# Kernel tuning notes

Hardware: AMD Instinct MI355X
Metric: run time of the kernel (lower is better)

The kernel has to match this reference:

```python
import jax, jax.numpy as jnp
import numpy as np

NH, NKV, HD = 32, 8, 128      # query heads, kv heads, head dim
B, S, H = 4, 1024, 4096       # batch, per-seq tokens (prefill, no history), hidden
BLOCK = 64                    # paged KV-cache block size
BPS = S // BLOCK              # blocks per sequence


def rotate_half(x):
    x1, x2 = jnp.split(x, 2, axis=-1)
    return jnp.concatenate([-x2, x1], axis=-1)


def setup_inputs() -> dict:
    key = jax.random.key(0)
    ks = jax.random.split(key, 5)
    hidden_states = jax.random.normal(ks[0], (B * S, H), jnp.float32)
    Wq = jax.random.normal(ks[1], (H, NH * HD), jnp.float32) * 0.02
    Wk = jax.random.normal(ks[2], (H, NKV * HD), jnp.float32) * 0.02
    Wv = jax.random.normal(ks[3], (H, NKV * HD), jnp.float32) * 0.02
    Wo = jax.random.normal(ks[4], (NH * HD, H), jnp.float32) * 0.02
    # standard llama rope inverse frequencies
    inv_freq = 1.0 / (10000.0 ** (jnp.arange(0, HD, 2, dtype=jnp.float32) / HD))
    # empty paged KV cache: [num_blocks, block, n_kv_heads, head_dim]
    k_cache = jnp.zeros((B * BPS, BLOCK, NKV, HD), jnp.float32)
    v_cache = jnp.zeros((B * BPS, BLOCK, NKV, HD), jnp.float32)
    # per-token positions (prefill, history=0): 0..S-1 for each sequence
    position_ids_1d = jnp.tile(jnp.arange(S, dtype=jnp.int32), B)
    # block table: which cache block holds each logical block of each sequence
    block_offsets = jnp.arange(B * BPS, dtype=jnp.int32).reshape(B, BPS)
    return dict(hidden_states=hidden_states, Wq=Wq, Wk=Wk, Wv=Wv, Wo=Wo,
                inv_freq=inv_freq, k_cache=k_cache, v_cache=v_cache,
                position_ids_1d=position_ids_1d, block_offsets=block_offsets)


def reference(hidden_states, Wq, Wk, Wv, Wo, inv_freq, k_cache, v_cache,
              position_ids_1d, block_offsets):
    # qkv projections (contiguous-batching: tokens flattened)
    q = (hidden_states @ Wq).reshape(-1, NH, HD)
    k = (hidden_states @ Wk).reshape(-1, NKV, HD)
    v = (hidden_states @ Wv).reshape(-1, NKV, HD)

    # fused rotary: cos/sin from inv_freq at per-token 1d positions
    freqs = position_ids_1d.astype(jnp.float32)[:, None] * inv_freq[None, :]  # [T, HD/2]
    emb = jnp.concatenate([freqs, freqs], axis=-1)                            # [T, HD]
    cos = jnp.cos(emb)[:, None, :]
    sin = jnp.sin(emb)[:, None, :]
    q = q * cos + rotate_half(q) * sin
    k = k * cos + rotate_half(k) * sin

    # fill_kv_cache: scatter rotated K / raw V into paged cache via block_offsets
    flat_offsets = block_offsets.reshape(-1)
    k_blk = k.reshape(B * BPS, BLOCK, NKV, HD)
    v_blk = v.reshape(B * BPS, BLOCK, NKV, HD)
    k_cache = k_cache.at[flat_offsets].set(k_blk)
    v_cache = v_cache.at[flat_offsets].set(v_blk)

    # paged_attention_fwd: gather K/V blocks back via block table
    kk = k_cache[block_offsets].reshape(B, BPS * BLOCK, NKV, HD)  # [B, Skv, NKV, HD]
    vv = v_cache[block_offsets].reshape(B, BPS * BLOCK, NKV, HD)
    groups = NH // NKV
    kk = jnp.repeat(kk, groups, axis=2)  # repeat_kv -> [B, Skv, NH, HD]
    vv = jnp.repeat(vv, groups, axis=2)

    qb = q.reshape(B, S, NH, HD)
    scale = 1.0 / jnp.sqrt(jnp.float32(HD))
    scores = jnp.einsum('bqhd,bkhd->bhqk', qb, kk) * scale  # [B, NH, S, Skv]
    causal = jnp.arange(S)[:, None] >= jnp.arange(BPS * BLOCK)[None, :]
    scores = jnp.where(causal[None, None], scores, jnp.float32(-1e30))
    probs = jax.nn.softmax(scores, axis=-1)
    attn = jnp.einsum('bhqk,bkhd->bqhd', probs, vv).reshape(B * S, NH * HD)
    return attn @ Wo
```

## Files before the change

kernel.cpp:

```cpp
#include <hip/hip_runtime.h>
#include <cstdint>
#include <cstddef>


typedef unsigned short u16;
typedef __bf16 bf16x8 __attribute__((ext_vector_type(8)));
typedef float  f32x4  __attribute__((ext_vector_type(4)));

#define SEQ 1024
#define QKV_COLS 6144
#define NHEAD 32
#define NKVH 8
#define HDIM 128

__device__ __forceinline__ u16 f2bf(float f) {
  union { float f; uint32_t u; } v; v.f = f;
  return (u16)((v.u + 0x7fffu + ((v.u >> 16) & 1u)) >> 16);
}
__device__ __forceinline__ float bf2f(u16 x) {
  union { uint32_t u; float f; } v; v.u = ((uint32_t)x) << 16;
  return v.f;
}

typedef __attribute__((address_space(1))) const uint32_t g_u32;
typedef __attribute__((address_space(3))) uint32_t l_u32;
__device__ __forceinline__ void async_copy16(const u16* g, u16* lds_base) {
  __builtin_amdgcn_global_load_lds((g_u32*)g, (l_u32*)lds_base, 16, 0, 0);
}

__global__ void cast_f32_bf16(const float* __restrict__ in, u16* __restrict__ out, int n) {
  int i = (blockIdx.x * 256 + threadIdx.x) * 4;
  if (i >= n) return;
  float4 v = *(const float4*)&in[i];
  uint2 pk;
  pk.x = (uint32_t)f2bf(v.x) | ((uint32_t)f2bf(v.y) << 16);
  pk.y = (uint32_t)f2bf(v.z) | ((uint32_t)f2bf(v.w) << 16);
  *(uint2*)&out[i] = pk;
}

__global__ void transpose_f32_bf16(const float* __restrict__ in, u16* __restrict__ out,
                                   int R, int C) {
  __shared__ float tile[32][33];
  int c0 = blockIdx.x * 32, r0 = blockIdx.y * 32;
  int tx = threadIdx.x, ty = threadIdx.y;
  tile[ty][tx] = in[(size_t)(r0 + ty) * C + c0 + tx];
  __syncthreads();
  out[(size_t)(c0 + ty) * R + r0 + tx] = f2bf(tile[tx][ty]);
}

template <int MODE>
__global__ __launch_bounds__(512, 2) void gemm_bt(const u16* __restrict__ A,
                                                  const u16* __restrict__ Bt,
                                                  void* __restrict__ Cv,
                                                  u16* __restrict__ Vt,
                                                  int M, int N, int K, int ldc,
                                                  int nbx) {
  __shared__ __align__(16) u16 smem[4][2][256 * 32];

  const int tid = threadIdx.x;
  const int lane = tid & 63, wave = tid >> 6;
  const int l15 = lane & 15, qd = lane >> 4;
  const int wm = wave >> 2, wn = wave & 3;

  const int nwg = gridDim.x;
  const int bid = (int)blockIdx.x;
  const int swz = (bid & 7) * (nwg >> 3) + (bid >> 3);
  const int bx = swz % nbx, by = swz / nbx;
  const int row0 = by * 256, col0 = bx * 256;

  const int sl = (qd ^ (l15 & 3) ^ (l15 >> 2)) * 8;

  int soff[2], cb[2];
#pragma unroll
  for (int call = 0; call < 2; ++call) {
    const int c = call * 512 + tid;
    const int r = c >> 2, j = c & 3;
    const int src = j ^ (r & 3) ^ ((r >> 2) & 3);
    soff[call] = r * K + src * 8;
    cb[call] = (call * 512 + wave * 64) * 8;
  }

  const u16* Ab = A + (size_t)row0 * K;
  const u16* Bb = Bt + (size_t)col0 * K;
  const int NT = K >> 5;

  f32x4 acc[8][4] = {};

#pragma unroll
  for (int tt = 0; tt < 3; ++tt) {
#pragma unroll
    for (int call = 0; call < 2; ++call)
      async_copy16(&Ab[tt * 32 + soff[call]], &smem[tt][0][cb[call]]);
#pragma unroll
    for (int call = 0; call < 2; ++call)
      async_copy16(&Bb[tt * 32 + soff[call]], &smem[tt][1][cb[call]]);
  }
  asm volatile("s_waitcnt vmcnt(4)" ::: "memory");
  __builtin_amdgcn_s_barrier();
  asm volatile("" ::: "memory");

  bf16x8 a0[4], b0[4];
#pragma unroll
  for (int i = 0; i < 4; ++i) {
    a0[i] = *(const bf16x8*)&smem[0][0][(wm * 128 + i * 16 + l15) * 32 + sl];
    b0[i] = *(const bf16x8*)&smem[0][1][(wn * 64 + i * 16 + l15) * 32 + sl];
  }

#pragma unroll 2
  for (int t = 0; t < NT; ++t) {
    const int bsel = t & 3, nsel = (t + 1) & 3, ssel = (t + 3) & 3;
    const bool do_stage = (t + 3) < NT;
    const int knext = (t + 3) * 32;

    bf16x8 a1[4];
#pragma unroll
    for (int i = 0; i < 4; ++i)
      a1[i] = *(const bf16x8*)&smem[bsel][0][(wm * 128 + 64 + i * 16 + l15) * 32 + sl];
    if (do_stage) {
#pragma unroll
      for (int call = 0; call < 2; ++call)
        async_copy16(&Ab[knext + soff[call]], &smem[ssel][0][cb[call]]);
    }
    __builtin_amdgcn_sched_barrier(0);
    __builtin_amdgcn_s_setprio(1);
#pragma unroll
    for (int mi = 0; mi < 4; ++mi)
#pragma unroll
      for (int ni = 0; ni < 4; ++ni)
        acc[mi][ni] = __builtin_amdgcn_mfma_f32_16x16x32_bf16(a0[mi], b0[ni], acc[mi][ni], 0, 0, 0);
    __builtin_amdgcn_s_setprio(0);

    bf16x8 a2[4], b2[4];
    if (t + 1 < NT) {
#pragma unroll
      for (int i = 0; i < 4; ++i) {
        a2[i] = *(const bf16x8*)&smem[nsel][0][(wm * 128 + i * 16 + l15) * 32 + sl];
        b2[i] = *(const bf16x8*)&smem[nsel][1][(wn * 64 + i * 16 + l15) * 32 + sl];
      }
    }
    if (do_stage) {
#pragma unroll
      for (int call = 0; call < 2; ++call)
        async_copy16(&Bb[knext + soff[call]], &smem[ssel][1][cb[call]]);
    }
    __builtin_amdgcn_sched_barrier(0);
    __builtin_amdgcn_s_setprio(1);
#pragma unroll
    for (int mi = 0; mi < 4; ++mi)
#pragma unroll
      for (int ni = 0; ni < 4; ++ni)
        acc[4 + mi][ni] = __builtin_amdgcn_mfma_f32_16x16x32_bf16(a1[mi], b0[ni], acc[4 + mi][ni], 0, 0, 0);
    __builtin_amdgcn_s_setprio(0);

    if (t < NT - 2) {
      if (t < NT - 3) asm volatile("s_waitcnt vmcnt(4)" ::: "memory");
      else            asm volatile("s_waitcnt vmcnt(0)" ::: "memory");
      __builtin_amdgcn_s_barrier();
      asm volatile("" ::: "memory");
    }
#pragma unroll
    for (int i = 0; i < 4; ++i) { a0[i] = a2[i]; b0[i] = b2[i]; }
  }

  if (MODE == 0 && col0 >= 5120) {
#pragma unroll
    for (int mi = 0; mi < 8; ++mi)
#pragma unroll
      for (int ni = 0; ni < 4; ++ni) {
        const int col = col0 + wn * 64 + ni * 16 + l15;
        const int dcol = col - 5120, kvh = dcol >> 7, d = dcol & 127;
        const int row = row0 + wm * 128 + mi * 16 + qd * 4;
        const int bb = row >> 10, p = row & 1023;
        ushort4 pk;
        pk.x = f2bf(acc[mi][ni][0]); pk.y = f2bf(acc[mi][ni][1]);
        pk.z = f2bf(acc[mi][ni][2]); pk.w = f2bf(acc[mi][ni][3]);
        *(ushort4*)&Vt[(((size_t)(bb * 8 + kvh) * 128) + d) * 1024 + p] = pk;
      }
    return;
  }
#pragma unroll
  for (int mi = 0; mi < 8; ++mi)
#pragma unroll
    for (int ni = 0; ni < 4; ++ni)
#pragma unroll
      for (int r = 0; r < 4; ++r) {
        int row = row0 + wm * 128 + mi * 16 + qd * 4 + r;
        int col = col0 + wn * 64 + ni * 16 + l15;
        float v = acc[mi][ni][r];
        if (MODE == 1) ((float*)Cv)[(size_t)row * ldc + col] = v;
        else           ((u16*)Cv)[(size_t)row * ldc + col] = f2bf(v);
      }
}

__global__ void rope_kernel(u16* __restrict__ qkv, const float* __restrict__ inv_freq,
                            const int* __restrict__ pos) {
  int idx = blockIdx.x * 256 + threadIdx.x;
  int t = idx / 2560;
  int r = idx - t * 2560;
  int hh = r >> 6, i = r & 63;
  float f = (float)pos[t] * inv_freq[i];
  float s, c;
  sincosf(f, &s, &c);
  size_t base = (size_t)t * QKV_COLS + hh * HDIM + i;
  float x1 = bf2f(qkv[base]), x2 = bf2f(qkv[base + 64]);
  qkv[base]      = f2bf(x1 * c - x2 * s);
  qkv[base + 64] = f2bf(x2 * c + x1 * s);
}

__global__ __launch_bounds__(512, 4) void attn_kernel(const u16* __restrict__ qkv,
                                                      const u16* __restrict__ vt,
                                                      u16* __restrict__ ao) {
  __shared__ __align__(16) u16 Ks[64 * 136];
  __shared__ __align__(16) u16 Vts[128 * 68];
  __shared__ __align__(16) u16 Ps[8][16 * 68];

  const int tid = threadIdx.x;
  const int lane = tid & 63, wave = tid >> 6;
  const int l15 = lane & 15, qd = lane >> 4;
  const int qt = blockIdx.x, h = blockIdx.y, b = blockIdx.z;
  const int q0 = qt * 128;
  const int kvh = h >> 2;
  const float scale = 0.08838834764831845f;

  bf16x8 qf[4];
  {
    const size_t qrow = (size_t)(b * SEQ + q0 + wave * 16 + l15) * QKV_COLS + h * HDIM;
#pragma unroll
    for (int s = 0; s < 4; ++s) qf[s] = *(const bf16x8*)&qkv[qrow + s * 32 + qd * 8];
  }

  f32x4 o[8] = {};
  float mrow[4] = {-__builtin_inff(), -__builtin_inff(), -__builtin_inff(), -__builtin_inff()};
  float lrow[4] = {0.f, 0.f, 0.f, 0.f};

  const int nkt = qt * 2 + 2;
  const size_t vbase0 = ((size_t)(b * NKVH + kvh) * HDIM) * SEQ;
  for (int kt = 0; kt < nkt; ++kt) {
    const int kv0 = kt * 64;
#pragma unroll
    for (int rnd = 0; rnd < 2; ++rnd) {
      int c = tid + rnd * 512;
      int kv = c >> 4, dc = (c & 15) * 8;
      *(uint4*)&Ks[kv * 136 + dc] =
          *(const uint4*)&qkv[(size_t)(b * SEQ + kv0 + kv) * QKV_COLS + 4096 + kvh * HDIM + dc];
    }
#pragma unroll
    for (int rnd = 0; rnd < 2; ++rnd) {
      int c = tid + rnd * 512;
      int d = c >> 3, kc = (c & 7) * 8;
      *(uint4*)&Vts[d * 68 + kc] = *(const uint4*)&vt[vbase0 + (size_t)d * SEQ + kv0 + kc];
    }
    __syncthreads();

    f32x4 st[4] = {};
#pragma unroll
    for (int t = 0; t < 4; ++t)
#pragma unroll
      for (int s = 0; s < 4; ++s) {
        bf16x8 kf = *(const bf16x8*)&Ks[(t * 16 + l15) * 136 + s * 32 + qd * 8];
        st[t] = __builtin_amdgcn_mfma_f32_16x16x32_bf16(qf[s], kf, st[t], 0, 0, 0);
      }

    float al[4];
#pragma unroll
    for (int r = 0; r < 4; ++r) {
      const int qpos = q0 + wave * 16 + qd * 4 + r;
      float sc[4];
#pragma unroll
      for (int t = 0; t < 4; ++t) {
        sc[t] = st[t][r] * scale;
        if (kv0 + t * 16 + l15 > qpos) sc[t] = -1e30f;
      }
      float mt = fmaxf(fmaxf(sc[0], sc[1]), fmaxf(sc[2], sc[3]));
      mt = fmaxf(mt, __shfl_xor(mt, 8));
      mt = fmaxf(mt, __shfl_xor(mt, 4));
      mt = fmaxf(mt, __shfl_xor(mt, 2));
      mt = fmaxf(mt, __shfl_xor(mt, 1));
      const float mn = fmaxf(mrow[r], mt);
      al[r] = __expf(mrow[r] - mn);
      float p[4], rs = 0.f;
#pragma unroll
      for (int t = 0; t < 4; ++t) { p[t] = __expf(sc[t] - mn); rs += p[t]; }
      rs += __shfl_xor(rs, 8);
      rs += __shfl_xor(rs, 4);
      rs += __shfl_xor(rs, 2);
      rs += __shfl_xor(rs, 1);
      lrow[r] = lrow[r] * al[r] + rs;
      mrow[r] = mn;
#pragma unroll
      for (int t = 0; t < 4; ++t)
        Ps[wave][(qd * 4 + r) * 68 + t * 16 + l15] = f2bf(p[t]);
    }
    asm volatile("s_waitcnt lgkmcnt(0)" ::: "memory");

    {
      const int srcl = (l15 >> 2) * 16;
      float a0 = __shfl(al[0], srcl), a1 = __shfl(al[1], srcl);
      float a2 = __shfl(al[2], srcl), a3 = __shfl(al[3], srcl);
      const int rr = l15 & 3;
      float aq = (rr & 2) ? ((rr & 1) ? a3 : a2) : ((rr & 1) ? a1 : a0);
#pragma unroll
      for (int dt = 0; dt < 8; ++dt) o[dt] *= aq;
    }
    {
      const bf16x8 pf0 = *(const bf16x8*)&Ps[wave][l15 * 68 + qd * 8];
      const bf16x8 pf1 = *(const bf16x8*)&Ps[wave][l15 * 68 + 32 + qd * 8];
#pragma unroll
      for (int dt = 0; dt < 8; ++dt) {
        const bf16x8 vf0 = *(const bf16x8*)&Vts[(dt * 16 + l15) * 68 + qd * 8];
        const bf16x8 vf1 = *(const bf16x8*)&Vts[(dt * 16 + l15) * 68 + 32 + qd * 8];
        o[dt] = __builtin_amdgcn_mfma_f32_16x16x32_bf16(vf0, pf0, o[dt], 0, 0, 0);
        o[dt] = __builtin_amdgcn_mfma_f32_16x16x32_bf16(vf1, pf1, o[dt], 0, 0, 0);
      }
    }
    __syncthreads();
  }

  {
    const int srcl = (l15 >> 2) * 16;
    float l0 = __shfl(lrow[0], srcl), l1 = __shfl(lrow[1], srcl);
    float l2 = __shfl(lrow[2], srcl), l3 = __shfl(lrow[3], srcl);
    const int rr = l15 & 3;
    float lq = (rr & 2) ? ((rr & 1) ? l3 : l2) : ((rr & 1) ? l1 : l0);
    const float inv = 1.0f / lq;
    const size_t obase = (size_t)(b * SEQ + q0 + wave * 16 + l15) * (NHEAD * HDIM) + h * HDIM;
#pragma unroll
    for (int dt = 0; dt < 8; ++dt) {
      ushort4 pk;
      pk.x = f2bf(o[dt][0] * inv); pk.y = f2bf(o[dt][1] * inv);
      pk.z = f2bf(o[dt][2] * inv); pk.w = f2bf(o[dt][3] * inv);
      *(ushort4*)&ao[obase + dt * 16 + qd * 4] = pk;
    }
  }
}

extern "C" void kernel_launch(void* const* d_in, const int* in_sizes, int n_in,
                              void* d_out, int out_size, void* d_ws, size_t ws_size,
                              hipStream_t stream) {
  const float* X    = (const float*)d_in[0];
  const float* Wq   = (const float*)d_in[1];
  const float* Wk   = (const float*)d_in[2];
  const float* Wv   = (const float*)d_in[3];
  const float* Wo   = (const float*)d_in[4];
  const float* invf = (const float*)d_in[5];
  const int*   pos  = (const int*)d_in[8];
  float* out = (float*)d_out;

  char* ws = (char*)d_ws;
  u16* Xbf   = (u16*)(ws + 0);
  u16* Wqkvt = (u16*)(ws + 33554432);
  u16* Wot   = (u16*)(ws + 83886080);
  u16* QKV   = (u16*)(ws + 117440512);
  u16* Vt    = (u16*)(ws + 167772160);
  u16* AO    = Xbf;

  dim3 tb32(32, 32);
  cast_f32_bf16<<<16384, 256, 0, stream>>>(X, Xbf, 16777216);
  transpose_f32_bf16<<<dim3(128, 128), tb32, 0, stream>>>(Wq, Wqkvt, 4096, 4096);
  transpose_f32_bf16<<<dim3(32, 128),  tb32, 0, stream>>>(Wk, Wqkvt + (size_t)4096 * 4096, 4096, 1024);
  transpose_f32_bf16<<<dim3(32, 128),  tb32, 0, stream>>>(Wv, Wqkvt + (size_t)5120 * 4096, 4096, 1024);
  transpose_f32_bf16<<<dim3(128, 128), tb32, 0, stream>>>(Wo, Wot, 4096, 4096);

  gemm_bt<0><<<dim3(24 * 16), 512, 0, stream>>>(Xbf, Wqkvt, QKV, Vt, 4096, 6144, 4096, 6144, 24);
  rope_kernel<<<40960, 256, 0, stream>>>(QKV, invf, pos);
  attn_kernel<<<dim3(8, 32, 4), 512, 0, stream>>>(QKV, Vt, AO);
  gemm_bt<1><<<dim3(16 * 16), 512, 0, stream>>>(AO, Wot, out, Vt, 4096, 4096, 4096, 4096, 16);
}
```

Before: 812.1 us.

## Fuse RoPE into QKV GEMM epilogue by retiling waves to cover full head dims

The GEMM wave layout changes from 2x4 (128 rows x 64 cols per wave) to 4x2 (64 rows x 128 cols per wave), so each wave holds a full 128-wide head and its rotate-half partner columns in registers. RoPE is then applied in the QKV GEMM epilogue using __sincosf, and the separate rope_kernel launch with its extra read-modify-write pass over Q/K is removed. The MFMA/LDS-read interleaving is reorganised to match the new tiling. The trade-offs are the less precise fast sincos, the transcendental work added to the epilogue, and a changed LDS read pattern.

```diff
diff --git a/kernel.cpp b/kernel.cpp
--- a/kernel.cpp
+++ b/kernel.cpp
@@ -53,6 +53,8 @@
                                                   const u16* __restrict__ Bt,
                                                   void* __restrict__ Cv,
                                                   u16* __restrict__ Vt,
+                                                  const float* __restrict__ invf,
+                                                  const int* __restrict__ pos,
                                                   int M, int N, int K, int ldc,
                                                   int nbx) {
   __shared__ __align__(16) u16 smem[4][2][256 * 32];
@@ -60,7 +62,7 @@
   const int tid = threadIdx.x;
   const int lane = tid & 63, wave = tid >> 6;
   const int l15 = lane & 15, qd = lane >> 4;
-  const int wm = wave >> 2, wn = wave & 3;
+  const int wm = wave & 3, wn = wave >> 2;
 
   const int nwg = gridDim.x;
   const int bid = (int)blockIdx.x;
@@ -84,7 +86,7 @@
   const u16* Bb = Bt + (size_t)col0 * K;
   const int NT = K >> 5;
 
-  f32x4 acc[8][4] = {};
+  f32x4 acc[4][8] = {};
 
 #pragma unroll
   for (int tt = 0; tt < 3; ++tt) {
@@ -99,23 +101,57 @@
   __builtin_amdgcn_s_barrier();
   asm volatile("" ::: "memory");
 
-  bf16x8 a0[4], b0[4];
+  bf16x8 a[4], b[4];
 #pragma unroll
   for (int i = 0; i < 4; ++i) {
-    a0[i] = *(const bf16x8*)&smem[0][0][(wm * 128 + i * 16 + l15) * 32 + sl];
-    b0[i] = *(const bf16x8*)&smem[0][1][(wn * 64 + i * 16 + l15) * 32 + sl];
+    a[i] = *(const bf16x8*)&smem[0][0][(wm * 64 + i * 16 + l15) * 32 + sl];
+    b[i] = *(const bf16x8*)&smem[0][1][(wn * 128 + i * 16 + l15) * 32 + sl];
   }
 
 #pragma unroll 2
   for (int t = 0; t < NT; ++t) {
     const int bsel = t & 3, nsel = (t + 1) & 3, ssel = (t + 3) & 3;
     const bool do_stage = (t + 3) < NT;
+    const bool have_next = (t + 1) < NT;
     const int knext = (t + 3) * 32;
-
-    bf16x8 a1[4];
+    const u16* Asc = &smem[bsel][0][0];
+    const u16* Bsc = &smem[bsel][1][0];
+    const u16* Asn = &smem[nsel][0][0];
+    const u16* Bsn = &smem[nsel][1][0];
+
+    bf16x8 bh[4];
 #pragma unroll
     for (int i = 0; i < 4; ++i)
-      a1[i] = *(const bf16x8*)&smem[bsel][0][(wm * 128 + 64 + i * 16 + l15) * 32 + sl];
+      bh[i] = *(const bf16x8*)&Bsc[(wn * 128 + (4 + i) * 16 + l15) * 32 + sl];
+    __builtin_amdgcn_sched_barrier(0);
+    __builtin_amdgcn_s_setprio(1);
+#pragma unroll
+    for (int mi = 0; mi < 2; ++mi)
+#pragma unroll
+      for (int ni = 0; ni < 4; ++ni)
+        acc[mi][ni] = __builtin_amdgcn_mfma_f32_16x16x32_bf16(a[mi], b[ni], acc[mi][ni], 0, 0, 0);
+    __builtin_amdgcn_s_setprio(0);
+
+    bf16x8 a2[4], b2[4];
+    if (have_next) {
+#pragma unroll
+      for (int i = 0; i < 4; ++i)
+        a2[i] = *(const bf16x8*)&Asn[(wm * 64 + i * 16 + l15) * 32 + sl];
+    }
+    __builtin_amdgcn_sched_barrier(0);
+    __builtin_amdgcn_s_setprio(1);
+#pragma unroll
+    for (int mi = 2; mi < 4; ++mi)
+#pragma unroll
+      for (int ni = 0; ni < 4; ++ni)
+        acc[mi][ni] = __builtin_amdgcn_mfma_f32_16x16x32_bf16(a[mi], b[ni], acc[mi][ni], 0, 0, 0);
+    __builtin_amdgcn_s_setprio(0);
+
+    if (have_next) {
+#pragma unroll
+      for (int i = 0; i < 4; ++i)
+        b2[i] = *(const bf16x8*)&Bsn[(wn * 128 + i * 16 + l15) * 32 + sl];
+    }
     if (do_stage) {
 #pragma unroll
       for (int call = 0; call < 2; ++call)
@@ -124,20 +160,12 @@
     __builtin_amdgcn_sched_barrier(0);
     __builtin_amdgcn_s_setprio(1);
 #pragma unroll
-    for (int mi = 0; mi < 4; ++mi)
+    for (int mi = 0; mi < 2; ++mi)
 #pragma unroll
       for (int ni = 0; ni < 4; ++ni)
-        acc[mi][ni] = __builtin_amdgcn_mfma_f32_16x16x32_bf16(a0[mi], b0[ni], acc[mi][ni], 0, 0, 0);
+        acc[mi][4 + ni] = __builtin_amdgcn_mfma_f32_16x16x32_bf16(a[mi], bh[ni], acc[mi][4 + ni], 0, 0, 0);
     __builtin_amdgcn_s_setprio(0);
 
-    bf16x8 a2[4], b2[4];
-    if (t + 1 < NT) {
-#pragma unroll
-      for (int i = 0; i < 4; ++i) {
-        a2[i] = *(const bf16x8*)&smem[nsel][0][(wm * 128 + i * 16 + l15) * 32 + sl];
-        b2[i] = *(const bf16x8*)&smem[nsel][1][(wn * 64 + i * 16 + l15) * 32 + sl];
-      }
-    }
     if (do_stage) {
 #pragma unroll
       for (int call = 0; call < 2; ++call)
@@ -146,10 +174,10 @@
     __builtin_amdgcn_sched_barrier(0);
     __builtin_amdgcn_s_setprio(1);
 #pragma unroll
-    for (int mi = 0; mi < 4; ++mi)
+    for (int mi = 2; mi < 4; ++mi)
 #pragma unroll
       for (int ni = 0; ni < 4; ++ni)
-        acc[4 + mi][ni] = __builtin_amdgcn_mfma_f32_16x16x32_bf16(a1[mi], b0[ni], acc[4 + mi][ni], 0, 0, 0);
+        acc[mi][4 + ni] = __builtin_amdgcn_mfma_f32_16x16x32_bf16(a[mi], bh[ni], acc[mi][4 + ni], 0, 0, 0);
     __builtin_amdgcn_s_setprio(0);
 
     if (t < NT - 2) {
@@ -158,18 +186,20 @@
       __builtin_amdgcn_s_barrier();
       asm volatile("" ::: "memory");
     }
-#pragma unroll
-    for (int i = 0; i < 4; ++i) { a0[i] = a2[i]; b0[i] = b2[i]; }
+    if (have_next) {
+#pragma unroll
+      for (int i = 0; i < 4; ++i) { a[i] = a2[i]; b[i] = b2[i]; }
+    }
   }
 
   if (MODE == 0 && col0 >= 5120) {
 #pragma unroll
-    for (int mi = 0; mi < 8; ++mi)
-#pragma unroll
-      for (int ni = 0; ni < 4; ++ni) {
-        const int col = col0 + wn * 64 + ni * 16 + l15;
+    for (int mi = 0; mi < 4; ++mi)
+#pragma unroll
+      for (int ni = 0; ni < 8; ++ni) {
+        const int col = col0 + wn * 128 + ni * 16 + l15;
         const int dcol = col - 5120, kvh = dcol >> 7, d = dcol & 127;
-        const int row = row0 + wm * 128 + mi * 16 + qd * 4;
+        const int row = row0 + wm * 64 + mi * 16 + qd * 4;
         const int bb = row >> 10, p = row & 1023;
         ushort4 pk;
         pk.x = f2bf(acc[mi][ni][0]); pk.y = f2bf(acc[mi][ni][1]);
@@ -178,33 +208,41 @@
       }
     return;
   }
-#pragma unroll
-  for (int mi = 0; mi < 8; ++mi)
-#pragma unroll
-    for (int ni = 0; ni < 4; ++ni)
+  if (MODE == 0) {
+    const int c0w = col0 + wn * 128;
+    float fi[4];
+#pragma unroll
+    for (int ni = 0; ni < 4; ++ni) fi[ni] = invf[ni * 16 + l15];
+    u16* C16 = (u16*)Cv;
+#pragma unroll
+    for (int mi = 0; mi < 4; ++mi) {
+      const int rbase = row0 + wm * 64 + mi * 16 + qd * 4;
 #pragma unroll
       for (int r = 0; r < 4; ++r) {
-        int row = row0 + wm * 128 + mi * 16 + qd * 4 + r;
-        int col = col0 + wn * 64 + ni * 16 + l15;
-        float v = acc[mi][ni][r];
-        if (MODE == 1) ((float*)Cv)[(size_t)row * ldc + col] = v;
-        else           ((u16*)Cv)[(size_t)row * ldc + col] = f2bf(v);
-      }
-}
-
-__global__ void rope_kernel(u16* __restrict__ qkv, const float* __restrict__ inv_freq,
-                            const int* __restrict__ pos) {
-  int idx = blockIdx.x * 256 + threadIdx.x;
-  int t = idx / 2560;
-  int r = idx - t * 2560;
-  int hh = r >> 6, i = r & 63;
-  float f = (float)pos[t] * inv_freq[i];
-  float s, c;
-  sincosf(f, &s, &c);
-  size_t base = (size_t)t * QKV_COLS + hh * HDIM + i;
-  float x1 = bf2f(qkv[base]), x2 = bf2f(qkv[base + 64]);
-  qkv[base]      = f2bf(x1 * c - x2 * s);
-  qkv[base + 64] = f2bf(x2 * c + x1 * s);
+        const float pv = (float)pos[rbase + r];
+        const size_t rowoff = (size_t)(rbase + r) * ldc + c0w;
+#pragma unroll
+        for (int ni = 0; ni < 4; ++ni) {
+          const float x1 = acc[mi][ni][r], x2 = acc[mi][ni + 4][r];
+          float s, c;
+          __sincosf(pv * fi[ni], &s, &c);
+          C16[rowoff + ni * 16 + l15]      = f2bf(x1 * c - x2 * s);
+          C16[rowoff + 64 + ni * 16 + l15] = f2bf(x2 * c + x1 * s);
+        }
+      }
+    }
+    return;
+  }
+#pragma unroll
+  for (int mi = 0; mi < 4; ++mi)
+#pragma unroll
+    for (int ni = 0; ni < 8; ++ni)
+#pragma unroll
+      for (int r = 0; r < 4; ++r) {
+        int row = row0 + wm * 64 + mi * 16 + qd * 4 + r;
+        int col = col0 + wn * 128 + ni * 16 + l15;
+        ((float*)Cv)[(size_t)row * ldc + col] = acc[mi][ni][r];
+      }
 }
 
 __global__ __launch_bounds__(512, 4) void attn_kernel(const u16* __restrict__ qkv,
@@ -361,8 +399,9 @@
   transpose_f32_bf16<<<dim3(32, 128),  tb32, 0, stream>>>(Wv, Wqkvt + (size_t)5120 * 4096, 4096, 1024);
   transpose_f32_bf16<<<dim3(128, 128), tb32, 0, stream>>>(Wo, Wot, 4096, 4096);
 
-  gemm_bt<0><<<dim3(24 * 16), 512, 0, stream>>>(Xbf, Wqkvt, QKV, Vt, 4096, 6144, 4096, 6144, 24);
-  rope_kernel<<<40960, 256, 0, stream>>>(QKV, invf, pos);
+  gemm_bt<0><<<dim3(24 * 16), 512, 0, stream>>>(Xbf, Wqkvt, QKV, Vt, invf, pos,
+                                                4096, 6144, 4096, 6144, 24);
   attn_kernel<<<dim3(8, 32, 4), 512, 0, stream>>>(QKV, Vt, AO);
-  gemm_bt<1><<<dim3(16 * 16), 512, 0, stream>>>(AO, Wot, out, Vt, 4096, 4096, 4096, 4096, 16);
-}
+  gemm_bt<1><<<dim3(16 * 16), 512, 0, stream>>>(AO, Wot, out, Vt, nullptr, nullptr,
+                                                4096, 4096, 4096, 4096, 16);
+}
```

Result: no change. 817.6 us (+0.7%).
